# Optimization experiments

Hardware: AMD Instinct MI355X
Metric: run time of the kernel (lower is better)

The kernel has to match this reference:

```python
import jax, jax.numpy as jnp
import numpy as np

EPS = 1e-6
ALPHA = 0.1
BETA = 0.25


def setup_inputs() -> dict:
    key = jax.random.key(0)
    k1, k2, k3 = jax.random.split(key, 3)
    B, C, D = 4096, 256, 128
    x = jax.random.normal(k1, (B, D), dtype=jnp.float32)
    prev_q = jax.random.normal(k2, (B, D), dtype=jnp.float32)
    codes = jax.random.normal(k3, (1, C, D), dtype=jnp.float32)
    return {"x": x, "prev_q": prev_q, "codes": codes}


def compute_distance(x, codes):
    # x: (B, D); codes: (1, C, D) or (B, 1, D) -> (B, C) / (B, 1); metric='l2'
    return jnp.sum((x[:, None, :] - codes) ** 2, axis=-1)


def get_rotation_matrix(u, v, eps=EPS):
    # u: (B, D) normalized; v: (D,) normalized -> R: (B, D, D)
    B, D = u.shape
    uvT = u[:, :, None] * v[None, None, :]          # (B, D, D) = u v^T
    vuT = v[None, :, None] * u[:, None, :]          # (B, D, D) = v u^T
    A = uvT - vuT
    A2 = jnp.einsum('bik,bkj->bij', A, A)
    dot = jnp.einsum('bd,d->b', u, v)[:, None, None]
    I = jnp.eye(D, dtype=u.dtype)
    return I + A + A2 / (1.0 + dot + eps)


def reference(x, prev_q, codes):
    B, D = x.shape
    v = jnp.ones((D,), dtype=x.dtype) / jnp.sqrt(jnp.asarray(D, x.dtype))
    # F.normalize(prev_q, dim=-1, eps=1e-6)
    n = jnp.linalg.norm(prev_q, axis=-1, keepdims=True)
    u = prev_q / jnp.maximum(n, EPS)
    R = get_rotation_matrix(u, v)
    # x_canonical = R^T x
    x_canonical = jnp.einsum('bji,bj->bi', R, x)
    raw_distances = compute_distance(x_canonical, codes)        # (B, C)
    distances = raw_distances / D / ALPHA
    # eval path: argmin + gather
    indices = jnp.argmin(distances, axis=-1)                    # (B,)
    quantized_canonical = codes[0][indices]                     # (B, D)
    quantized = jnp.einsum('bij,bj->bi', R, quantized_canonical)
    loss_commit = compute_distance(x, jax.lax.stop_gradient(quantized)[:, None, :]).mean()
    loss_codebook = compute_distance(jax.lax.stop_gradient(x), quantized[:, None, :]).mean()
    loss = loss_commit + BETA * loss_codebook
    return quantized, indices, loss
```

## Files before the change

kernel.cpp:

```cpp
#include <hip/hip_runtime.h>

#define BD 4096
#define CD 256
#define DD 128
#define RB 16
#define TB 1024
#define SF 132

__global__ __launch_bounds__(TB) void rq_fused(
    const float* __restrict__ x,
    const float* __restrict__ pq,
    const float* __restrict__ codes,
    float* __restrict__ out)
{
    __shared__ __align__(16) char pool[CD * SF * 4
                                       + RB * DD * 4
                                       + CD * 4
                                       + RB * 4 * 4
                                       + RB * 4
                                       + RB * 2 * 8
                                       + RB * 4];
    float* code_s = (float*)pool;
    float* mbuf   = (float*)pool;
    float* xc_s   = (float*)(pool + CD * SF * 4);
    float* cn2_s  = xc_s + RB * DD;
    float* row_c  = cn2_s + CD;
    float* row_s  = row_c + RB;
    float* row_invn = row_s + RB;
    float* row_pad  = row_invn + RB;  (void)row_pad;
    int*   row_idx  = (int*)(row_invn + 2 * RB);
    float* red_v    = (float*)(row_idx + RB);
    int*   red_i    = (int*)(red_v + RB * 2);
    float* loss_s   = (float*)(red_i + RB * 2);

    const int tid  = threadIdx.x;
    const int wv   = tid >> 6;
    const int lane = tid & 63;
    const int row0 = blockIdx.x * RB;
    const float INV_SQRT_D = 0.088388347648318447f;

    const size_t growA = (size_t)(row0 + wv);
    const float2 xv = ((const float2*)(x  + growA * DD))[lane];
    const float2 pv = ((const float2*)(pq + growA * DD))[lane];

    {
        const float4* src = (const float4*)codes;
        #pragma unroll
        for (int k = 0; k < 8; k += 4) {
            const float4 t0 = src[(k + 0) * TB + tid];
            const float4 t1 = src[(k + 1) * TB + tid];
            const float4 t2 = src[(k + 2) * TB + tid];
            const float4 t3 = src[(k + 3) * TB + tid];
            int f;
            f = (k + 0) * TB + tid; *(float4*)(code_s + (f >> 5) * SF + (f & 31) * 4) = t0;
            f = (k + 1) * TB + tid; *(float4*)(code_s + (f >> 5) * SF + (f & 31) * 4) = t1;
            f = (k + 2) * TB + tid; *(float4*)(code_s + (f >> 5) * SF + (f & 31) * 4) = t2;
            f = (k + 3) * TB + tid; *(float4*)(code_s + (f >> 5) * SF + (f & 31) * 4) = t3;
        }
    }

    {
        const int r = wv;
        float s0 = pv.x * pv.x + pv.y * pv.y;
        float s1 = pv.x + pv.y;
        float s2 = xv.x + xv.y;
        float s3 = pv.x * xv.x + pv.y * xv.y;
        #pragma unroll
        for (int m = 32; m > 0; m >>= 1) {
            s0 += __shfl_xor(s0, m);
            s1 += __shfl_xor(s1, m);
            s2 += __shfl_xor(s2, m);
            s3 += __shfl_xor(s3, m);
        }
        const float invn = 1.0f / fmaxf(sqrtf(s0), 1e-6f);
        const float b = s2 * INV_SQRT_D;
        const float a = s3 * invn;
        const float c = s1 * invn * INV_SQRT_D;
        const float s = 1.0f / (1.0f + c + 1e-6f);
        const float au = -b + s * (c * b - a);
        const float av =  a + s * (c * a - b);
        float2 o;
        o.x = xv.x + au * (pv.x * invn) + av * INV_SQRT_D;
        o.y = xv.y + au * (pv.y * invn) + av * INV_SQRT_D;
        ((float2*)(xc_s + r * DD))[lane] = o;
        if (lane == 0) { row_c[r] = c; row_s[r] = s; row_invn[r] = invn; }
    }
    __syncthreads();

    {
        const int c = tid >> 2, q = tid & 3;
        const float* cp = code_s + c * SF + q * 32;
        float n2 = 0.f;
        #pragma unroll
        for (int i = 0; i < 8; ++i) {
            const float4 v = *(const float4*)(cp + i * 4);
            n2 = fmaf(v.x, v.x, n2); n2 = fmaf(v.y, v.y, n2);
            n2 = fmaf(v.z, v.z, n2); n2 = fmaf(v.w, v.w, n2);
        }
        n2 += __shfl_xor(n2, 1);
        n2 += __shfl_xor(n2, 2);
        if (q == 0) cn2_s[c] = n2;
    }
    __syncthreads();

    const int wgrp = wv & 7, half = wv >> 3;
    const int rg = wgrp & 3, ch = wgrp >> 2;
    const float* cb = code_s + (ch * 128 + lane) * SF + half * 64;
    float xreg[4];
    #pragma unroll
    for (int rr = 0; rr < 4; ++rr)
        xreg[rr] = xc_s[(rg * 4 + rr) * DD + half * 64 + lane];
    float a0 = 0.f, a1 = 0.f, a2 = 0.f, a3 = 0.f;
    float a4 = 0.f, a5 = 0.f, a6 = 0.f, a7 = 0.f;

    #define RL(rr, j) __int_as_float(__builtin_amdgcn_readlane(__float_as_int(xreg[rr]), (j)))
    #pragma unroll
    for (int i = 0; i < 16; ++i) {
        const float4 c0 = *(const float4*)(cb + i * 4);
        const float4 c1 = *(const float4*)(cb + 64 * SF + i * 4);
        const float x00 = RL(0, 4 * i + 0), x01 = RL(0, 4 * i + 1);
        const float x02 = RL(0, 4 * i + 2), x03 = RL(0, 4 * i + 3);
        const float x10 = RL(1, 4 * i + 0), x11 = RL(1, 4 * i + 1);
        const float x12 = RL(1, 4 * i + 2), x13 = RL(1, 4 * i + 3);
        const float x20 = RL(2, 4 * i + 0), x21 = RL(2, 4 * i + 1);
        const float x22 = RL(2, 4 * i + 2), x23 = RL(2, 4 * i + 3);
        const float x30 = RL(3, 4 * i + 0), x31 = RL(3, 4 * i + 1);
        const float x32 = RL(3, 4 * i + 2), x33 = RL(3, 4 * i + 3);
        a0 = fmaf(c0.x, x00, a0); a0 = fmaf(c0.y, x01, a0);
        a0 = fmaf(c0.z, x02, a0); a0 = fmaf(c0.w, x03, a0);
        a1 = fmaf(c1.x, x00, a1); a1 = fmaf(c1.y, x01, a1);
        a1 = fmaf(c1.z, x02, a1); a1 = fmaf(c1.w, x03, a1);
        a2 = fmaf(c0.x, x10, a2); a2 = fmaf(c0.y, x11, a2);
        a2 = fmaf(c0.z, x12, a2); a2 = fmaf(c0.w, x13, a2);
        a3 = fmaf(c1.x, x10, a3); a3 = fmaf(c1.y, x11, a3);
        a3 = fmaf(c1.z, x12, a3); a3 = fmaf(c1.w, x13, a3);
        a4 = fmaf(c0.x, x20, a4); a4 = fmaf(c0.y, x21, a4);
        a4 = fmaf(c0.z, x22, a4); a4 = fmaf(c0.w, x23, a4);
        a5 = fmaf(c1.x, x20, a5); a5 = fmaf(c1.y, x21, a5);
        a5 = fmaf(c1.z, x22, a5); a5 = fmaf(c1.w, x23, a5);
        a6 = fmaf(c0.x, x30, a6); a6 = fmaf(c0.y, x31, a6);
        a6 = fmaf(c0.z, x32, a6); a6 = fmaf(c0.w, x33, a6);
        a7 = fmaf(c1.x, x30, a7); a7 = fmaf(c1.y, x31, a7);
        a7 = fmaf(c1.z, x32, a7); a7 = fmaf(c1.w, x33, a7);
    }
    #undef RL

    __syncthreads();
    if (half == 1) {
        float* mb = mbuf + ((size_t)wgrp * 64 + lane) * 8;
        float4 v;
        v.x = a0; v.y = a1; v.z = a2; v.w = a3; *(float4*)(mb)     = v;
        v.x = a4; v.y = a5; v.z = a6; v.w = a7; *(float4*)(mb + 4) = v;
    }
    __syncthreads();
    if (half == 0) {
        const float* mb = mbuf + ((size_t)wgrp * 64 + lane) * 8;
        const float4 m0 = *(const float4*)(mb);
        const float4 m1 = *(const float4*)(mb + 4);
        a0 += m0.x; a1 += m0.y; a2 += m0.z; a3 += m0.w;
        a4 += m1.x; a5 += m1.y; a6 += m1.z; a7 += m1.w;
        const int c0i = ch * 128 + lane;
        const int c1i = c0i + 64;
        const float cn20 = cn2_s[c0i];
        const float cn21 = cn2_s[c1i];
        float bv[4]; int bi[4];
        {
            const float s00 = fmaf(-2.f, a0, cn20), s01 = fmaf(-2.f, a1, cn21);
            const float s10 = fmaf(-2.f, a2, cn20), s11 = fmaf(-2.f, a3, cn21);
            const float s20 = fmaf(-2.f, a4, cn20), s21 = fmaf(-2.f, a5, cn21);
            const float s30 = fmaf(-2.f, a6, cn20), s31 = fmaf(-2.f, a7, cn21);
            if (s01 < s00) { bv[0] = s01; bi[0] = c1i; } else { bv[0] = s00; bi[0] = c0i; }
            if (s11 < s10) { bv[1] = s11; bi[1] = c1i; } else { bv[1] = s10; bi[1] = c0i; }
            if (s21 < s20) { bv[2] = s21; bi[2] = c1i; } else { bv[2] = s20; bi[2] = c0i; }
            if (s31 < s30) { bv[3] = s31; bi[3] = c1i; } else { bv[3] = s30; bi[3] = c0i; }
        }
        #pragma unroll
        for (int m = 1; m < 64; m <<= 1) {
            #pragma unroll
            for (int rr = 0; rr < 4; ++rr) {
                const float ov = __shfl_xor(bv[rr], m);
                const int   oi = __shfl_xor(bi[rr], m);
                if (ov < bv[rr] || (ov == bv[rr] && oi < bi[rr])) { bv[rr] = ov; bi[rr] = oi; }
            }
        }
        if (lane == 0) {
            #pragma unroll
            for (int rr = 0; rr < 4; ++rr) {
                red_v[(rg * 4 + rr) * 2 + ch] = bv[rr];
                red_i[(rg * 4 + rr) * 2 + ch] = bi[rr];
            }
        }
    }
    __syncthreads();
    if (tid < RB) {
        float v0 = red_v[tid * 2]; int i0 = red_i[tid * 2];
        const float v1 = red_v[tid * 2 + 1]; const int i1 = red_i[tid * 2 + 1];
        if (v1 < v0 || (v1 == v0 && i1 < i0)) { v0 = v1; i0 = i1; }
        row_idx[tid] = i0;
        out[(size_t)BD * DD + row0 + tid] = (float)i0;
    }
    __syncthreads();

    {
        const int r = wv;
        const int qi = row_idx[r];
        const float invn = row_invn[r];
        const float c = row_c[r];
        const float s = row_s[r];
        const size_t grow = growA;
        const float2 q = ((const float2*)(codes + (size_t)qi * DD))[lane];
        float pd = pv.x * q.x + pv.y * q.y;
        float ws = q.x + q.y;
        #pragma unroll
        for (int m = 32; m > 0; m >>= 1) {
            pd += __shfl_xor(pd, m);
            ws += __shfl_xor(ws, m);
        }
        const float pp = pd * invn;
        const float w  = ws * INV_SQRT_D;
        const float bu  =  w + s * (c * w - pp);
        const float bvv = -pp + s * (c * pp - w);
        float2 o;
        o.x = q.x + bu * (pv.x * invn) + bvv * INV_SQRT_D;
        o.y = q.y + bu * (pv.y * invn) + bvv * INV_SQRT_D;
        ((float2*)(out + grow * DD))[lane] = o;

        float dx = xv.x - o.x;
        float ls = dx * dx;
        dx = xv.y - o.y;
        ls = fmaf(dx, dx, ls);
        #pragma unroll
        for (int m = 32; m > 0; m >>= 1) ls += __shfl_xor(ls, m);
        if (lane == 0) loss_s[r] = ls;
    }
    __syncthreads();
    if (tid == 0) {
        float tot = 0.f;
        #pragma unroll
        for (int r = 0; r < RB; ++r) tot += loss_s[r];
        atomicAdd(out + (size_t)BD * DD + BD, tot * (1.25f / (float)BD));
    }
}

extern "C" void kernel_launch(void* const* d_in, const int* in_sizes, int n_in,
                              void* d_out, int out_size, void* d_ws, size_t ws_size,
                              hipStream_t stream) {
    const float* xin   = (const float*)d_in[0];
    const float* prevq = (const float*)d_in[1];
    const float* codes = (const float*)d_in[2];
    float* out = (float*)d_out;
    rq_fused<<<BD / RB, TB, 0, stream>>>(xin, prevq, codes, out);
}
```

Before: 74.15 us.

## Load codebook via direct global-to-LDS with XOR swizzle and split D into quarters

Codebook staging now uses global_load_lds DMA straight into shared memory, replacing the padded register round-trip, and an XOR swizzle replaces the padding to avoid bank conflicts. The distance matmul is repartitioned so each wave handles all 256 codes for a quarter of the D dimension, with a 4-way partial-sum reduction through LDS. The per-row argmin then finishes inside one wave, which removes the second cross-wave reduction and one barrier. It risks more LDS traffic in the partial-sum merge, and the builtin's width and swizzle must line up exactly for correctness.

```diff
diff --git a/kernel.cpp b/kernel.cpp
--- a/kernel.cpp
+++ b/kernel.cpp
@@ -5,7 +5,6 @@
 #define DD 128
 #define RB 16
 #define TB 1024
-#define SF 132
 
 __global__ __launch_bounds__(TB) void rq_fused(
     const float* __restrict__ x,
@@ -13,25 +12,21 @@
     const float* __restrict__ codes,
     float* __restrict__ out)
 {
-    __shared__ __align__(16) char pool[CD * SF * 4
+    __shared__ __align__(16) char pool[CD * DD * 4
                                        + RB * DD * 4
                                        + CD * 4
                                        + RB * 4 * 4
                                        + RB * 4
-                                       + RB * 2 * 8
                                        + RB * 4];
-    float* code_s = (float*)pool;
-    float* mbuf   = (float*)pool;
-    float* xc_s   = (float*)(pool + CD * SF * 4);
-    float* cn2_s  = xc_s + RB * DD;
-    float* row_c  = cn2_s + CD;
-    float* row_s  = row_c + RB;
-    float* row_invn = row_s + RB;
-    float* row_pad  = row_invn + RB;  (void)row_pad;
-    int*   row_idx  = (int*)(row_invn + 2 * RB);
-    float* red_v    = (float*)(row_idx + RB);
-    int*   red_i    = (int*)(red_v + RB * 2);
-    float* loss_s   = (float*)(red_i + RB * 2);
+    float*  code_s = (float*)pool;
+    float4* mb4    = (float4*)pool;
+    float*  xc_s   = (float*)(pool + CD * DD * 4);
+    float*  cn2_s  = xc_s + RB * DD;
+    float*  row_c  = cn2_s + CD;
+    float*  row_s  = row_c + RB;
+    float*  row_invn = row_s + RB;
+    int*    row_idx  = (int*)(row_invn + 2 * RB);
+    float*  loss_s   = (float*)(row_idx + RB);
 
     const int tid  = threadIdx.x;
     const int wv   = tid >> 6;
@@ -44,18 +39,14 @@
     const float2 pv = ((const float2*)(pq + growA * DD))[lane];
 
     {
-        const float4* src = (const float4*)codes;
-        #pragma unroll
-        for (int k = 0; k < 8; k += 4) {
-            const float4 t0 = src[(k + 0) * TB + tid];
-            const float4 t1 = src[(k + 1) * TB + tid];
-            const float4 t2 = src[(k + 2) * TB + tid];
-            const float4 t3 = src[(k + 3) * TB + tid];
-            int f;
-            f = (k + 0) * TB + tid; *(float4*)(code_s + (f >> 5) * SF + (f & 31) * 4) = t0;
-            f = (k + 1) * TB + tid; *(float4*)(code_s + (f >> 5) * SF + (f & 31) * 4) = t1;
-            f = (k + 2) * TB + tid; *(float4*)(code_s + (f >> 5) * SF + (f & 31) * 4) = t2;
-            f = (k + 3) * TB + tid; *(float4*)(code_s + (f >> 5) * SF + (f & 31) * 4) = t3;
+        #pragma unroll
+        for (int k = 0; k < 8; ++k) {
+            const int f = k * TB + tid;
+            const int g = f ^ ((f >> 5) & 7);
+            __builtin_amdgcn_global_load_lds(
+                (const __attribute__((address_space(1))) uint32_t*)(codes + (size_t)g * 4),
+                (__attribute__((address_space(3))) uint32_t*)(code_s + (size_t)f * 4),
+                16, 0, 0);
         }
     }
 
@@ -89,11 +80,12 @@
 
     {
         const int c = tid >> 2, q = tid & 3;
-        const float* cp = code_s + c * SF + q * 32;
+        const int sw = c & 7;
+        const float* cp = code_s + c * DD + q * 32;
         float n2 = 0.f;
         #pragma unroll
         for (int i = 0; i < 8; ++i) {
-            const float4 v = *(const float4*)(cp + i * 4);
+            const float4 v = *(const float4*)(cp + ((i ^ sw) << 2));
             n2 = fmaf(v.x, v.x, n2); n2 = fmaf(v.y, v.y, n2);
             n2 = fmaf(v.z, v.z, n2); n2 = fmaf(v.w, v.w, n2);
         }
@@ -103,101 +95,91 @@
     }
     __syncthreads();
 
-    const int wgrp = wv & 7, half = wv >> 3;
-    const int rg = wgrp & 3, ch = wgrp >> 2;
-    const float* cb = code_s + (ch * 128 + lane) * SF + half * 64;
+    const int rg = wv & 3, dq = wv >> 2;
     float xreg[4];
     #pragma unroll
     for (int rr = 0; rr < 4; ++rr)
-        xreg[rr] = xc_s[(rg * 4 + rr) * DD + half * 64 + lane];
-    float a0 = 0.f, a1 = 0.f, a2 = 0.f, a3 = 0.f;
-    float a4 = 0.f, a5 = 0.f, a6 = 0.f, a7 = 0.f;
-
+        xreg[rr] = xc_s[(rg * 4 + rr) * DD + dq * 32 + (lane & 31)];
+    const int sw = lane & 7;
+    const float* cb = code_s + lane * DD + dq * 32;
+    float acc[4][4] = {};
     #define RL(rr, j) __int_as_float(__builtin_amdgcn_readlane(__float_as_int(xreg[rr]), (j)))
     #pragma unroll
-    for (int i = 0; i < 16; ++i) {
-        const float4 c0 = *(const float4*)(cb + i * 4);
-        const float4 c1 = *(const float4*)(cb + 64 * SF + i * 4);
-        const float x00 = RL(0, 4 * i + 0), x01 = RL(0, 4 * i + 1);
-        const float x02 = RL(0, 4 * i + 2), x03 = RL(0, 4 * i + 3);
-        const float x10 = RL(1, 4 * i + 0), x11 = RL(1, 4 * i + 1);
-        const float x12 = RL(1, 4 * i + 2), x13 = RL(1, 4 * i + 3);
-        const float x20 = RL(2, 4 * i + 0), x21 = RL(2, 4 * i + 1);
-        const float x22 = RL(2, 4 * i + 2), x23 = RL(2, 4 * i + 3);
-        const float x30 = RL(3, 4 * i + 0), x31 = RL(3, 4 * i + 1);
-        const float x32 = RL(3, 4 * i + 2), x33 = RL(3, 4 * i + 3);
-        a0 = fmaf(c0.x, x00, a0); a0 = fmaf(c0.y, x01, a0);
-        a0 = fmaf(c0.z, x02, a0); a0 = fmaf(c0.w, x03, a0);
-        a1 = fmaf(c1.x, x00, a1); a1 = fmaf(c1.y, x01, a1);
-        a1 = fmaf(c1.z, x02, a1); a1 = fmaf(c1.w, x03, a1);
-        a2 = fmaf(c0.x, x10, a2); a2 = fmaf(c0.y, x11, a2);
-        a2 = fmaf(c0.z, x12, a2); a2 = fmaf(c0.w, x13, a2);
-        a3 = fmaf(c1.x, x10, a3); a3 = fmaf(c1.y, x11, a3);
-        a3 = fmaf(c1.z, x12, a3); a3 = fmaf(c1.w, x13, a3);
-        a4 = fmaf(c0.x, x20, a4); a4 = fmaf(c0.y, x21, a4);
-        a4 = fmaf(c0.z, x22, a4); a4 = fmaf(c0.w, x23, a4);
-        a5 = fmaf(c1.x, x20, a5); a5 = fmaf(c1.y, x21, a5);
-        a5 = fmaf(c1.z, x22, a5); a5 = fmaf(c1.w, x23, a5);
-        a6 = fmaf(c0.x, x30, a6); a6 = fmaf(c0.y, x31, a6);
-        a6 = fmaf(c0.z, x32, a6); a6 = fmaf(c0.w, x33, a6);
-        a7 = fmaf(c1.x, x30, a7); a7 = fmaf(c1.y, x31, a7);
-        a7 = fmaf(c1.z, x32, a7); a7 = fmaf(c1.w, x33, a7);
+    for (int i = 0; i < 8; ++i) {
+        const int off = (i ^ sw) << 2;
+        const float4 c0 = *(const float4*)(cb + off);
+        const float4 c1 = *(const float4*)(cb +  64 * DD + off);
+        const float4 c2 = *(const float4*)(cb + 128 * DD + off);
+        const float4 c3 = *(const float4*)(cb + 192 * DD + off);
+        #pragma unroll
+        for (int r = 0; r < 4; ++r) {
+            const float y0 = RL(r, 4 * i + 0), y1 = RL(r, 4 * i + 1);
+            const float y2 = RL(r, 4 * i + 2), y3 = RL(r, 4 * i + 3);
+            acc[0][r] = fmaf(c0.x, y0, acc[0][r]); acc[0][r] = fmaf(c0.y, y1, acc[0][r]);
+            acc[0][r] = fmaf(c0.z, y2, acc[0][r]); acc[0][r] = fmaf(c0.w, y3, acc[0][r]);
+            acc[1][r] = fmaf(c1.x, y0, acc[1][r]); acc[1][r] = fmaf(c1.y, y1, acc[1][r]);
+            acc[1][r] = fmaf(c1.z, y2, acc[1][r]); acc[1][r] = fmaf(c1.w, y3, acc[1][r]);
+            acc[2][r] = fmaf(c2.x, y0, acc[2][r]); acc[2][r] = fmaf(c2.y, y1, acc[2][r]);
+            acc[2][r] = fmaf(c2.z, y2, acc[2][r]); acc[2][r] = fmaf(c2.w, y3, acc[2][r]);
+            acc[3][r] = fmaf(c3.x, y0, acc[3][r]); acc[3][r] = fmaf(c3.y, y1, acc[3][r]);
+            acc[3][r] = fmaf(c3.z, y2, acc[3][r]); acc[3][r] = fmaf(c3.w, y3, acc[3][r]);
+        }
     }
     #undef RL
 
     __syncthreads();
-    if (half == 1) {
-        float* mb = mbuf + ((size_t)wgrp * 64 + lane) * 8;
-        float4 v;
-        v.x = a0; v.y = a1; v.z = a2; v.w = a3; *(float4*)(mb)     = v;
-        v.x = a4; v.y = a5; v.z = a6; v.w = a7; *(float4*)(mb + 4) = v;
-    }
-    __syncthreads();
-    if (half == 0) {
-        const float* mb = mbuf + ((size_t)wgrp * 64 + lane) * 8;
-        const float4 m0 = *(const float4*)(mb);
-        const float4 m1 = *(const float4*)(mb + 4);
-        a0 += m0.x; a1 += m0.y; a2 += m0.z; a3 += m0.w;
-        a4 += m1.x; a5 += m1.y; a6 += m1.z; a7 += m1.w;
-        const int c0i = ch * 128 + lane;
-        const int c1i = c0i + 64;
-        const float cn20 = cn2_s[c0i];
-        const float cn21 = cn2_s[c1i];
+    if (dq != 0) {
+        const int e = (rg * 3 + (dq - 1)) * 64 + lane;
+        #pragma unroll
+        for (int t = 0; t < 4; ++t) {
+            float4 w;
+            w.x = acc[t][0]; w.y = acc[t][1]; w.z = acc[t][2]; w.w = acc[t][3];
+            mb4[t * 768 + e] = w;
+        }
+    }
+    __syncthreads();
+    if (dq == 0) {
+        #pragma unroll
+        for (int s = 0; s < 3; ++s) {
+            const int e = (rg * 3 + s) * 64 + lane;
+            #pragma unroll
+            for (int t = 0; t < 4; ++t) {
+                const float4 pm = mb4[t * 768 + e];
+                acc[t][0] += pm.x; acc[t][1] += pm.y; acc[t][2] += pm.z; acc[t][3] += pm.w;
+            }
+        }
+        const float cn0  = cn2_s[lane];
+        const float cn1  = cn2_s[lane + 64];
+        const float cn2v = cn2_s[lane + 128];
+        const float cn3  = cn2_s[lane + 192];
         float bv[4]; int bi[4];
-        {
-            const float s00 = fmaf(-2.f, a0, cn20), s01 = fmaf(-2.f, a1, cn21);
-            const float s10 = fmaf(-2.f, a2, cn20), s11 = fmaf(-2.f, a3, cn21);
-            const float s20 = fmaf(-2.f, a4, cn20), s21 = fmaf(-2.f, a5, cn21);
-            const float s30 = fmaf(-2.f, a6, cn20), s31 = fmaf(-2.f, a7, cn21);
-            if (s01 < s00) { bv[0] = s01; bi[0] = c1i; } else { bv[0] = s00; bi[0] = c0i; }
-            if (s11 < s10) { bv[1] = s11; bi[1] = c1i; } else { bv[1] = s10; bi[1] = c0i; }
-            if (s21 < s20) { bv[2] = s21; bi[2] = c1i; } else { bv[2] = s20; bi[2] = c0i; }
-            if (s31 < s30) { bv[3] = s31; bi[3] = c1i; } else { bv[3] = s30; bi[3] = c0i; }
+        #pragma unroll
+        for (int r = 0; r < 4; ++r) {
+            float v0 = fmaf(-2.f, acc[0][r], cn0); int i0 = lane;
+            const float v1 = fmaf(-2.f, acc[1][r], cn1);
+            const float v2 = fmaf(-2.f, acc[2][r], cn2v);
+            const float v3 = fmaf(-2.f, acc[3][r], cn3);
+            if (v1 < v0) { v0 = v1; i0 = lane + 64;  }
+            if (v2 < v0) { v0 = v2; i0 = lane + 128; }
+            if (v3 < v0) { v0 = v3; i0 = lane + 192; }
+            bv[r] = v0; bi[r] = i0;
         }
         #pragma unroll
         for (int m = 1; m < 64; m <<= 1) {
             #pragma unroll
-            for (int rr = 0; rr < 4; ++rr) {
-                const float ov = __shfl_xor(bv[rr], m);
-                const int   oi = __shfl_xor(bi[rr], m);
-                if (ov < bv[rr] || (ov == bv[rr] && oi < bi[rr])) { bv[rr] = ov; bi[rr] = oi; }
+            for (int r = 0; r < 4; ++r) {
+                const float ov = __shfl_xor(bv[r], m);
+                const int   oi = __shfl_xor(bi[r], m);
+                if (ov < bv[r] || (ov == bv[r] && oi < bi[r])) { bv[r] = ov; bi[r] = oi; }
             }
         }
         if (lane == 0) {
             #pragma unroll
-            for (int rr = 0; rr < 4; ++rr) {
-                red_v[(rg * 4 + rr) * 2 + ch] = bv[rr];
-                red_i[(rg * 4 + rr) * 2 + ch] = bi[rr];
+            for (int r = 0; r < 4; ++r) {
+                row_idx[rg * 4 + r] = bi[r];
+                out[(size_t)BD * DD + row0 + rg * 4 + r] = (float)bi[r];
             }
         }
-    }
-    __syncthreads();
-    if (tid < RB) {
-        float v0 = red_v[tid * 2]; int i0 = red_i[tid * 2];
-        const float v1 = red_v[tid * 2 + 1]; const int i1 = red_i[tid * 2 + 1];
-        if (v1 < v0 || (v1 == v0 && i1 < i0)) { v0 = v1; i0 = i1; }
-        row_idx[tid] = i0;
-        out[(size_t)BD * DD + row0 + tid] = (float)i0;
     }
     __syncthreads();
 
@@ -207,7 +189,6 @@
         const float invn = row_invn[r];
         const float c = row_c[r];
         const float s = row_s[r];
-        const size_t grow = growA;
         const float2 q = ((const float2*)(codes + (size_t)qi * DD))[lane];
         float pd = pv.x * q.x + pv.y * q.y;
         float ws = q.x + q.y;
@@ -223,7 +204,7 @@
         float2 o;
         o.x = q.x + bu * (pv.x * invn) + bvv * INV_SQRT_D;
         o.y = q.y + bu * (pv.y * invn) + bvv * INV_SQRT_D;
-        ((float2*)(out + grow * DD))[lane] = o;
+        ((float2*)(out + growA * DD))[lane] = o;
 
         float dx = xv.x - o.x;
         float ls = dx * dx;
```

New measurement: 74.63 us. About the same (+0.6%).
